# Kernel optimization log

Hardware: AMD Instinct MI355X
Metric: run time of the kernel (lower is better)

## Reference

```python
import jax, jax.numpy as jnp
import numpy as np

UNITS = 2048
INPUT_DIM = 2048
BATCH = 8192


def setup_inputs() -> dict:
    key = jax.random.key(0)
    k_x, k_w = jax.random.split(key)
    inputs = jax.random.normal(k_x, (BATCH, INPUT_DIM), dtype=jnp.float32)
    # random_normal initializer in keras defaults to stddev=0.05
    w = jax.random.normal(k_w, (INPUT_DIM, UNITS), dtype=jnp.float32) * 0.05
    b = jnp.zeros((UNITS,), dtype=jnp.float32)
    return {"inputs": inputs, "w": w, "b": b}


def reference(inputs, w, b):
    # matmul + bias
    result = jnp.matmul(inputs, w) + b  # [B, units]
    # per-row: if first element > 0.5, add 1 to whole row, else subtract 1
    cond = result[:, :1] > 0.5  # [B, 1], broadcasts over row
    return jnp.where(cond, result + 1.0, result - 1.0)
```

## Files before the change

### kernel.cpp

```cpp
#include <hip/hip_runtime.h>
#include <hip/hip_bf16.h>
#include <stdint.h>

#define M_DIM 8192
#define N_DIM 2048
#define K_DIM 2048

typedef __attribute__((ext_vector_type(8))) short bf16x8;
typedef __attribute__((ext_vector_type(8))) short short8;
typedef __attribute__((ext_vector_type(4))) float f32x4;

static __device__ __forceinline__ unsigned short f2bf(float f) {
  union { float f; unsigned u; } a; a.f = f;
  unsigned u = a.u;
  u += 0x7FFFu + ((u >> 16) & 1u);
  return (unsigned short)(u >> 16);
}

static __device__ __forceinline__ void async16(void* lds, const void* g) {
  __builtin_amdgcn_global_load_lds(
      (const __attribute__((address_space(1))) unsigned int*)g,
      (__attribute__((address_space(3))) unsigned int*)lds, 16, 0, 0);
}

#define BAR()                                \
  do {                                       \
    asm volatile("" ::: "memory");           \
    __builtin_amdgcn_s_barrier();            \
    asm volatile("" ::: "memory");           \
  } while (0)
#define VMCNT(n) asm volatile("s_waitcnt vmcnt(" #n ")" ::: "memory")

__global__ __launch_bounds__(256) void k_wcol(const float* __restrict__ W,
                                              float* __restrict__ wcol) {
  int k = blockIdx.x * 256 + threadIdx.x;
  if (k < K_DIM) wcol[k] = W[(size_t)k * N_DIM];
}

__global__ __launch_bounds__(256) void k_convX(const float* __restrict__ X,
    const float* __restrict__ wcol, const float* __restrict__ b,
    unsigned short* __restrict__ Xb, float* __restrict__ adj) {
  const int m = blockIdx.x;
  const int t = threadIdx.x;
  const float4* xr = (const float4*)(X + (size_t)m * K_DIM);
  const float4* wc = (const float4*)wcol;
  float4 x0 = xr[2 * t], x1 = xr[2 * t + 1];
  float4 w0 = wc[2 * t], w1 = wc[2 * t + 1];
  short8 o;
  o[0] = (short)f2bf(x0.x); o[1] = (short)f2bf(x0.y);
  o[2] = (short)f2bf(x0.z); o[3] = (short)f2bf(x0.w);
  o[4] = (short)f2bf(x1.x); o[5] = (short)f2bf(x1.y);
  o[6] = (short)f2bf(x1.z); o[7] = (short)f2bf(x1.w);
  *(short8*)(Xb + (size_t)m * K_DIM + t * 8) = o;
  double s = (double)x0.x * w0.x + (double)x0.y * w0.y +
             (double)x0.z * w0.z + (double)x0.w * w0.w +
             (double)x1.x * w1.x + (double)x1.y * w1.y +
             (double)x1.z * w1.z + (double)x1.w * w1.w;
  #pragma unroll
  for (int off = 32; off > 0; off >>= 1) s += __shfl_down(s, off, 64);
  __shared__ double red[4];
  if ((t & 63) == 0) red[t >> 6] = s;
  __syncthreads();
  if (t == 0) {
    double tot = red[0] + red[1] + red[2] + red[3] + (double)b[0];
    adj[m] = (tot > 0.5) ? 1.0f : -1.0f;
  }
}

__global__ __launch_bounds__(256) void k_transW(const float* __restrict__ W,
                                                unsigned short* __restrict__ Wt) {
  __shared__ float tile[64][65];
  const int bx = blockIdx.x & 31;
  const int by = blockIdx.x >> 5;
  const int n0 = bx * 64, k0 = by * 64;
  const int t = threadIdx.x;
  #pragma unroll
  for (int i = 0; i < 16; ++i) {
    int lin = i * 256 + t;
    int r = lin >> 6, c = lin & 63;
    tile[r][c] = W[(size_t)(k0 + r) * N_DIM + n0 + c];
  }
  __syncthreads();
  #pragma unroll
  for (int i = 0; i < 16; ++i) {
    int lin = i * 256 + t;
    int r = lin >> 6, c = lin & 63;
    Wt[(size_t)(n0 + r) * K_DIM + k0 + c] = f2bf(tile[c][r]);
  }
}

__device__ __forceinline__ void stage_unit(char* ldsc,
    const unsigned short* __restrict__ src, int row0, int kt,
    int isB, int sel, int wid, int l) {
  char* base = ldsc + (size_t)(kt & 1) * 65536 + (size_t)isB * 32768;
  #pragma unroll
  for (int j = 0; j < 2; ++j) {
    int s = wid * 2 + j;
    int sub_c = s & 1;
    int idx = s >> 1;
    int sub_r = isB ? ((idx & 1) + (idx >> 1) * 4 + sel * 2)
                    : ((idx & 3) + ((idx & 4) ? 8 : 0) + sel * 4);
    int grow = row0 + sub_r * 16 + (l >> 2);
    int gcol = kt * 64 + sub_c * 32 + (((l & 3) * 8) ^ ((l & 32) >> 1));
    async16(base + (size_t)(sub_r * 2 + sub_c) * 1024,
            src + (size_t)grow * K_DIM + gcol);
  }
}

__global__ __launch_bounds__(512, 1) void k_gemm8(
    const unsigned short* __restrict__ A,
    const unsigned short* __restrict__ B,
    const float* __restrict__ bias,
    const float* __restrict__ adj,
    float* __restrict__ out) {
  __shared__ unsigned short lds[2 * 2 * 256 * 64];
  char* ldsc = (char*)lds;

  const int t = threadIdx.x;
  const int wid = t >> 6, l = t & 63;
  const int wm = wid >> 2, wn = wid & 3;

  const int bid = blockIdx.x;
  const int swz = (bid & 7) * 32 + (bid >> 3);
  const int bm = swz >> 3, bn = swz & 7;
  const int m0 = bm * 256, n0 = bn * 256;

  const int r = l & 15, q = l >> 4;
  const int rdoff = (r * 64 + q * 16) ^ ((r & 8) << 2);

  f32x4 acc[8][4] = {};

#define STG(isB, sel, kt) \
  stage_unit(ldsc, (isB) ? B : A, (isB) ? n0 : m0, kt, isB, sel, wid, l)

#define RD_A(MH)                                                           \
  _Pragma("unroll") for (int mi4 = 0; mi4 < 4; ++mi4) {                    \
    const int sub_r = wm * 8 + (MH) * 4 + mi4;                             \
    _Pragma("unroll") for (int ks = 0; ks < 2; ++ks)                       \
      af[ks][mi4] =                                                        \
          *(const bf16x8*)(ab + (size_t)(sub_r * 2 + ks) * 1024 + rdoff);  \
  }

#define RD_B(DST, NH)                                                      \
  _Pragma("unroll") for (int ni2 = 0; ni2 < 2; ++ni2) {                    \
    const int sub_r = wn * 4 + (NH) * 2 + ni2;                             \
    _Pragma("unroll") for (int ks = 0; ks < 2; ++ks)                       \
      DST[ks][ni2] =                                                       \
          *(const bf16x8*)(bb + (size_t)(sub_r * 2 + ks) * 1024 + rdoff);  \
  }

#define PHASE(BUF, MH, NH, READ_STMT, STAGE_STMT, WAIT_STMT)               \
  {                                                                        \
    const char* ab = ldsc + (size_t)(BUF) * 65536;                         \
    const char* bb = ab + 32768;                                           \
    (void)ab; (void)bb;                                                    \
    READ_STMT;                                                             \
    STAGE_STMT;                                                            \
    BAR();                                                                 \
    __builtin_amdgcn_s_setprio(1);                                         \
    _Pragma("unroll") for (int ks = 0; ks < 2; ++ks)                       \
      _Pragma("unroll") for (int mi4 = 0; mi4 < 4; ++mi4)                  \
        _Pragma("unroll") for (int ni2 = 0; ni2 < 2; ++ni2) {              \
          const int mi = (MH) * 4 + mi4, ni = (NH) * 2 + ni2;              \
          acc[mi][ni] = __builtin_amdgcn_mfma_f32_16x16x32_bf16(           \
              af[ks][mi4], ((NH) ? bv1 : bv0)[ks][ni2], acc[mi][ni],       \
              0, 0, 0);                                                    \
        }                                                                  \
    __builtin_amdgcn_s_setprio(0);                                         \
    WAIT_STMT;                                                             \
    BAR();                                                                 \
  }

  STG(0, 0, 0); STG(1, 0, 0); STG(1, 1, 0); STG(0, 1, 0);
  VMCNT(2);
  BAR();

  for (int j = 0; j < 31; ++j) {
    const int buf = j & 1;
    const int nt = j + 1;
    bf16x8 af[2][4], bv0[2][2], bv1[2][2];
    PHASE(buf, 0, 0, RD_A(0); RD_B(bv0, 0); RD_B(bv1, 1),
          STG(0, 0, nt), );
    PHASE(buf, 0, 1, , STG(1, 0, nt), VMCNT(4));
    PHASE(buf, 1, 0, RD_A(1), STG(1, 1, nt), );
    PHASE(buf, 1, 1, , STG(0, 1, nt), VMCNT(2));
  }
  {
    bf16x8 af[2][4], bv0[2][2], bv1[2][2];
    PHASE(1, 0, 0, RD_A(0); RD_B(bv0, 0); RD_B(bv1, 1), , );
    PHASE(1, 0, 1, , , VMCNT(0));
    PHASE(1, 1, 0, RD_A(1), , );
    PHASE(1, 1, 1, , , );
  }

#undef PHASE
#undef RD_A
#undef RD_B
#undef STG

  #pragma unroll
  for (int mi = 0; mi < 8; ++mi) {
    const int rowb = m0 + wm * 128 + mi * 16 + q * 4;
    float adjv[4];
    #pragma unroll
    for (int j = 0; j < 4; ++j) adjv[j] = adj[rowb + j];
    #pragma unroll
    for (int ni = 0; ni < 4; ++ni) {
      const int col = n0 + wn * 64 + ni * 16 + r;
      const float bvs = bias[col];
      #pragma unroll
      for (int j = 0; j < 4; ++j)
        out[(size_t)(rowb + j) * N_DIM + col] = acc[mi][ni][j] + bvs + adjv[j];
    }
  }
}

__global__ __launch_bounds__(256) void k_gemm_f32(const float* __restrict__ X,
    const float* __restrict__ W, const float* __restrict__ b,
    float* __restrict__ out) {
  __shared__ float As[16][16];
  __shared__ float Bs[16][17];
  const int bn = blockIdx.x & 127, bm = blockIdx.x >> 7;
  const int tx = threadIdx.x & 15, ty = threadIdx.x >> 4;
  const int row = bm * 16 + ty, col = bn * 16 + tx;
  float acc = 0.f;
  for (int k0 = 0; k0 < K_DIM; k0 += 16) {
    As[ty][tx] = X[(size_t)row * K_DIM + k0 + tx];
    Bs[ty][tx] = W[(size_t)(k0 + ty) * N_DIM + col];
    __syncthreads();
    #pragma unroll
    for (int kk = 0; kk < 16; ++kk) acc += As[ty][kk] * Bs[kk][tx];
    __syncthreads();
  }
  out[(size_t)row * N_DIM + col] = acc + b[col];
}

__global__ __launch_bounds__(256) void k_rowadj(float* __restrict__ out) {
  const int m = blockIdx.x;
  const float c0 = out[(size_t)m * N_DIM];
  __syncthreads();
  const float a = (c0 > 0.5f) ? 1.0f : -1.0f;
  for (int n = threadIdx.x; n < N_DIM; n += 256)
    out[(size_t)m * N_DIM + n] += a;
}

extern "C" void kernel_launch(void* const* d_in, const int* in_sizes, int n_in,
                              void* d_out, int out_size, void* d_ws, size_t ws_size,
                              hipStream_t stream) {
  const float* X = (const float*)d_in[0];
  const float* W = (const float*)d_in[1];
  const float* b = (const float*)d_in[2];
  float* out = (float*)d_out;

  const size_t XB_OFF   = 0;
  const size_t WT_OFF   = (size_t)M_DIM * K_DIM * 2;
  const size_t ADJ_OFF  = WT_OFF + (size_t)N_DIM * K_DIM * 2;
  const size_t WCOL_OFF = ADJ_OFF + (size_t)M_DIM * 4;
  const size_t NEED     = WCOL_OFF + (size_t)K_DIM * 4;

  if (ws_size >= NEED) {
    unsigned short* Xb  = (unsigned short*)((char*)d_ws + XB_OFF);
    unsigned short* Wt  = (unsigned short*)((char*)d_ws + WT_OFF);
    float* adj  = (float*)((char*)d_ws + ADJ_OFF);
    float* wcol = (float*)((char*)d_ws + WCOL_OFF);
    k_wcol<<<dim3(8), dim3(256), 0, stream>>>(W, wcol);
    k_convX<<<dim3(M_DIM), dim3(256), 0, stream>>>(X, wcol, b, Xb, adj);
    k_transW<<<dim3(1024), dim3(256), 0, stream>>>(W, Wt);
    k_gemm8<<<dim3((M_DIM / 256) * (N_DIM / 256)), dim3(512), 0, stream>>>(
        Xb, Wt, b, adj, out);
  } else {
    k_gemm_f32<<<dim3((M_DIM / 16) * (N_DIM / 16)), dim3(256), 0, stream>>>(
        X, W, b, out);
    k_rowadj<<<dim3(M_DIM), dim3(256), 0, stream>>>(out);
  }
}
```

Baseline: 93.20 us.

## Switch GEMM to 32x32x16 MFMA tiles and fold wcol extraction into transpose

The main GEMM now issues mfma_f32_32x32x16_bf16 on 32x32 accumulator blocks instead of 16x16x32, with new LDS read addressing and a matching epilogue that loads adj as float4. The larger MFMA shape halves the instruction count and improves operand reuse per LDS read. Separately, the W column-0 extraction is folded into the transpose kernel, which removes one launch. The risks are LDS bank conflicts under the new read pattern and higher accumulator register pressure.

```diff
diff --git a/kernel.cpp b/kernel.cpp
--- a/kernel.cpp
+++ b/kernel.cpp
@@ -9,6 +9,7 @@
 typedef __attribute__((ext_vector_type(8))) short bf16x8;
 typedef __attribute__((ext_vector_type(8))) short short8;
 typedef __attribute__((ext_vector_type(4))) float f32x4;
+typedef __attribute__((ext_vector_type(16))) float f32x16;
 
 static __device__ __forceinline__ unsigned short f2bf(float f) {
   union { float f; unsigned u; } a; a.f = f;
@@ -31,10 +32,29 @@
   } while (0)
 #define VMCNT(n) asm volatile("s_waitcnt vmcnt(" #n ")" ::: "memory")
 
-__global__ __launch_bounds__(256) void k_wcol(const float* __restrict__ W,
-                                              float* __restrict__ wcol) {
-  int k = blockIdx.x * 256 + threadIdx.x;
-  if (k < K_DIM) wcol[k] = W[(size_t)k * N_DIM];
+__global__ __launch_bounds__(256) void k_transW(const float* __restrict__ W,
+                                                unsigned short* __restrict__ Wt,
+                                                float* __restrict__ wcol) {
+  __shared__ float tile[64][65];
+  const int bx = blockIdx.x & 31;
+  const int by = blockIdx.x >> 5;
+  const int n0 = bx * 64, k0 = by * 64;
+  const int t = threadIdx.x;
+  #pragma unroll
+  for (int i = 0; i < 16; ++i) {
+    int lin = i * 256 + t;
+    int r = lin >> 6, c = lin & 63;
+    float v = W[(size_t)(k0 + r) * N_DIM + n0 + c];
+    tile[r][c] = v;
+    if (bx == 0 && c == 0) wcol[k0 + r] = v;
+  }
+  __syncthreads();
+  #pragma unroll
+  for (int i = 0; i < 16; ++i) {
+    int lin = i * 256 + t;
+    int r = lin >> 6, c = lin & 63;
+    Wt[(size_t)(n0 + r) * K_DIM + k0 + c] = f2bf(tile[c][r]);
+  }
 }
 
 __global__ __launch_bounds__(256) void k_convX(const float* __restrict__ X,
@@ -67,28 +87,6 @@
   }
 }
 
-__global__ __launch_bounds__(256) void k_transW(const float* __restrict__ W,
-                                                unsigned short* __restrict__ Wt) {
-  __shared__ float tile[64][65];
-  const int bx = blockIdx.x & 31;
-  const int by = blockIdx.x >> 5;
-  const int n0 = bx * 64, k0 = by * 64;
-  const int t = threadIdx.x;
-  #pragma unroll
-  for (int i = 0; i < 16; ++i) {
-    int lin = i * 256 + t;
-    int r = lin >> 6, c = lin & 63;
-    tile[r][c] = W[(size_t)(k0 + r) * N_DIM + n0 + c];
-  }
-  __syncthreads();
-  #pragma unroll
-  for (int i = 0; i < 16; ++i) {
-    int lin = i * 256 + t;
-    int r = lin >> 6, c = lin & 63;
-    Wt[(size_t)(n0 + r) * K_DIM + k0 + c] = f2bf(tile[c][r]);
-  }
-}
-
 __device__ __forceinline__ void stage_unit(char* ldsc,
     const unsigned short* __restrict__ src, int row0, int kt,
     int isB, int sel, int wid, int l) {
@@ -125,50 +123,52 @@
   const int bm = swz >> 3, bn = swz & 7;
   const int m0 = bm * 256, n0 = bn * 256;
 
-  const int r = l & 15, q = l >> 4;
-  const int rdoff = (r * 64 + q * 16) ^ ((r & 8) << 2);
-
-  f32x4 acc[8][4] = {};
+  const int lane_sub = ((l & 31) >> 4) * 2048;
+  const int lane_row = (l & 15) * 64;
+  const int lane_kc  = (l >> 5) * 16;
+  const int lane_swz = (l & 8) << 2;
+
+  f32x16 acc[4][2] = {};
 
 #define STG(isB, sel, kt) \
   stage_unit(ldsc, (isB) ? B : A, (isB) ? n0 : m0, kt, isB, sel, wid, l)
 
-#define RD_A(MH)                                                           \
-  _Pragma("unroll") for (int mi4 = 0; mi4 < 4; ++mi4) {                    \
-    const int sub_r = wm * 8 + (MH) * 4 + mi4;                             \
-    _Pragma("unroll") for (int ks = 0; ks < 2; ++ks)                       \
-      af[ks][mi4] =                                                        \
-          *(const bf16x8*)(ab + (size_t)(sub_r * 2 + ks) * 1024 + rdoff);  \
-  }
-
-#define RD_B(DST, NH)                                                      \
-  _Pragma("unroll") for (int ni2 = 0; ni2 < 2; ++ni2) {                    \
-    const int sub_r = wn * 4 + (NH) * 2 + ni2;                             \
-    _Pragma("unroll") for (int ks = 0; ks < 2; ++ks)                       \
-      DST[ks][ni2] =                                                       \
-          *(const bf16x8*)(bb + (size_t)(sub_r * 2 + ks) * 1024 + rdoff);  \
-  }
-
-#define PHASE(BUF, MH, NH, READ_STMT, STAGE_STMT, WAIT_STMT)               \
-  {                                                                        \
-    const char* ab = ldsc + (size_t)(BUF) * 65536;                         \
-    const char* bb = ab + 32768;                                           \
-    (void)ab; (void)bb;                                                    \
-    READ_STMT;                                                             \
-    STAGE_STMT;                                                            \
-    BAR();                                                                 \
-    __builtin_amdgcn_s_setprio(1);                                         \
-    _Pragma("unroll") for (int ks = 0; ks < 2; ++ks)                       \
-      _Pragma("unroll") for (int mi4 = 0; mi4 < 4; ++mi4)                  \
-        _Pragma("unroll") for (int ni2 = 0; ni2 < 2; ++ni2) {              \
-          const int mi = (MH) * 4 + mi4, ni = (NH) * 2 + ni2;              \
-          acc[mi][ni] = __builtin_amdgcn_mfma_f32_16x16x32_bf16(           \
-              af[ks][mi4], ((NH) ? bv1 : bv0)[ks][ni2], acc[mi][ni],       \
-              0, 0, 0);                                                    \
-        }                                                                  \
-    __builtin_amdgcn_s_setprio(0);                                         \
-    WAIT_STMT;                                                             \
-    BAR();                                                                 \
+#define RD_A(MH)                                                            \
+  _Pragma("unroll") for (int mb2 = 0; mb2 < 2; ++mb2) {                     \
+    const char* abase = ab + ((size_t)(wm * 8 + ((MH) * 2 + mb2) * 2)) *    \
+                                 2048 + lane_sub + lane_row;                \
+    _Pragma("unroll") for (int ks = 0; ks < 4; ++ks)                        \
+      af[mb2][ks] = *(const bf16x8*)(abase + (ks >> 1) * 1024 +             \
+                        ((((ks & 1) * 32) + lane_kc) ^ lane_swz));          \
+  }
+
+#define RD_B(DST, NH)                                                       \
+  {                                                                         \
+    const char* bbase = bb + ((size_t)(wn * 4 + (NH) * 2)) * 2048 +         \
+                        lane_sub + lane_row;                                \
+    _Pragma("unroll") for (int ks = 0; ks < 4; ++ks)                        \
+      DST[ks] = *(const bf16x8*)(bbase + (ks >> 1) * 1024 +                 \
+                    ((((ks & 1) * 32) + lane_kc) ^ lane_swz));              \
+  }
+
+#define PHASE(BUF, MH, NH, READ_STMT, STAGE_STMT, WAIT_STMT)                \
+  {                                                                         \
+    const char* ab = ldsc + (size_t)(BUF) * 65536;                          \
+    const char* bb = ab + 32768;                                            \
+    (void)ab; (void)bb;                                                     \
+    READ_STMT;                                                              \
+    STAGE_STMT;                                                             \
+    BAR();                                                                  \
+    __builtin_amdgcn_s_setprio(1);                                          \
+    _Pragma("unroll") for (int ks = 0; ks < 4; ++ks)                        \
+      _Pragma("unroll") for (int mb2 = 0; mb2 < 2; ++mb2) {                 \
+        acc[(MH) * 2 + mb2][NH] = __builtin_amdgcn_mfma_f32_32x32x16_bf16(  \
+            af[mb2][ks], ((NH) ? bv1 : bv0)[ks], acc[(MH) * 2 + mb2][NH],   \
+            0, 0, 0);                                                       \
+      }                                                                     \
+    __builtin_amdgcn_s_setprio(0);                                          \
+    WAIT_STMT;                                                              \
+    BAR();                                                                  \
   }
 
   STG(0, 0, 0); STG(1, 0, 0); STG(1, 1, 0); STG(0, 1, 0);
@@ -178,7 +178,7 @@
   for (int j = 0; j < 31; ++j) {
     const int buf = j & 1;
     const int nt = j + 1;
-    bf16x8 af[2][4], bv0[2][2], bv1[2][2];
+    bf16x8 af[2][4], bv0[4], bv1[4];
     PHASE(buf, 0, 0, RD_A(0); RD_B(bv0, 0); RD_B(bv1, 1),
           STG(0, 0, nt), );
     PHASE(buf, 0, 1, , STG(1, 0, nt), VMCNT(4));
@@ -186,7 +186,7 @@
     PHASE(buf, 1, 1, , STG(0, 1, nt), VMCNT(2));
   }
   {
-    bf16x8 af[2][4], bv0[2][2], bv1[2][2];
+    bf16x8 af[2][4], bv0[4], bv1[4];
     PHASE(1, 0, 0, RD_A(0); RD_B(bv0, 0); RD_B(bv1, 1), , );
     PHASE(1, 0, 1, , , VMCNT(0));
     PHASE(1, 1, 0, RD_A(1), , );
@@ -199,18 +199,20 @@
 #undef STG
 
   #pragma unroll
-  for (int mi = 0; mi < 8; ++mi) {
-    const int rowb = m0 + wm * 128 + mi * 16 + q * 4;
-    float adjv[4];
+  for (int mb = 0; mb < 4; ++mb) {
     #pragma unroll
-    for (int j = 0; j < 4; ++j) adjv[j] = adj[rowb + j];
-    #pragma unroll
-    for (int ni = 0; ni < 4; ++ni) {
-      const int col = n0 + wn * 64 + ni * 16 + r;
+    for (int nb = 0; nb < 2; ++nb) {
+      const int col = n0 + wn * 64 + nb * 32 + (l & 31);
       const float bvs = bias[col];
       #pragma unroll
-      for (int j = 0; j < 4; ++j)
-        out[(size_t)(rowb + j) * N_DIM + col] = acc[mi][ni][j] + bvs + adjv[j];
+      for (int rg = 0; rg < 4; ++rg) {
+        const int rowb = m0 + wm * 128 + mb * 32 + rg * 8 + 4 * (l >> 5);
+        const float4 adjv = *(const float4*)&adj[rowb];
+        #pragma unroll
+        for (int rr = 0; rr < 4; ++rr)
+          out[(size_t)(rowb + rr) * N_DIM + col] =
+              acc[mb][nb][rg * 4 + rr] + bvs + adjv[rr];
+      }
     }
   }
 }
@@ -263,9 +265,8 @@
     unsigned short* Wt  = (unsigned short*)((char*)d_ws + WT_OFF);
     float* adj  = (float*)((char*)d_ws + ADJ_OFF);
     float* wcol = (float*)((char*)d_ws + WCOL_OFF);
-    k_wcol<<<dim3(8), dim3(256), 0, stream>>>(W, wcol);
+    k_transW<<<dim3(1024), dim3(256), 0, stream>>>(W, Wt, wcol);
     k_convX<<<dim3(M_DIM), dim3(256), 0, stream>>>(X, wcol, b, Xb, adj);
-    k_transW<<<dim3(1024), dim3(256), 0, stream>>>(W, Wt);
     k_gemm8<<<dim3((M_DIM / 256) * (N_DIM / 256)), dim3(512), 0, stream>>>(
         Xb, Wt, b, adj, out);
   } else {
```

After: 102.9 us. 1.1x slower.
